# Kernel tuning notes

Hardware: AMD Instinct MI355X
Metric: run time of the kernel (lower is better)

## Reference

```python
import jax, jax.numpy as jnp
import numpy as np

N = 50000
E = 800000
IN_DIM = 16
H = 128
L = 4
EDGE_DIM = 7
LN_EPS = 1e-5


def _linear_params(key, fan_in, fan_out):
    kw, kb = jax.random.split(key)
    w = jax.random.normal(kw, (fan_in, fan_out), jnp.float32) * 0.02
    b = jax.random.normal(kb, (fan_out,), jnp.float32) * 0.02
    return w, b


def setup_inputs() -> dict:
    key = jax.random.key(0)
    ks = jax.random.split(key, 20)
    x = jax.random.normal(ks[0], (N, IN_DIM), jnp.float32)
    pos = jax.random.uniform(ks[1], (N, 3), jnp.float32) * 10.0
    row = jax.random.randint(ks[2], (E,), 0, N, jnp.int32)
    # guarantee no self-loops so distance > 0 (radius_graph uses loop=False)
    off = jax.random.randint(ks[3], (E,), 1, N, jnp.int32)
    col = (row + off) % N
    edge_index = jnp.stack([row, col], axis=0)

    W_in, b_in = _linear_params(ks[4], IN_DIM, H)

    def stack_layers(kbase, fan_in, fan_out):
        ws, bs = [], []
        for l in range(L):
            w, b = _linear_params(jax.random.fold_in(kbase, l), fan_in, fan_out)
            ws.append(w); bs.append(b)
        return jnp.stack(ws), jnp.stack(bs)

    We1, be1 = stack_layers(ks[5], 2 * H + EDGE_DIM, H)
    We2, be2 = stack_layers(ks[6], H, H)
    We3, be3 = stack_layers(ks[7], H, H)
    Wn1, bn1 = stack_layers(ks[8], H + H, H)
    Wn2, bn2 = stack_layers(ks[9], H, H)
    Wn3, bn3 = stack_layers(ks[10], H, H)
    ln_g = jnp.ones((L, H), jnp.float32)
    ln_b = jnp.zeros((L, H), jnp.float32)

    return {
        'x': x, 'pos': pos, 'edge_index': edge_index,
        'W_in': W_in, 'b_in': b_in,
        'We1': We1, 'be1': be1, 'We2': We2, 'be2': be2, 'We3': We3, 'be3': be3,
        'Wn1': Wn1, 'bn1': bn1, 'Wn2': Wn2, 'bn2': bn2, 'Wn3': Wn3, 'bn3': bn3,
        'ln_g': ln_g, 'ln_b': ln_b,
    }


def reference(x, pos, edge_index, W_in, b_in, We1, be1, We2, be2, We3, be3,
              Wn1, bn1, Wn2, bn2, Wn3, bn3, ln_g, ln_b):
    n = x.shape[0]
    row, col = edge_index[0], edge_index[1]  # row=source, col=target (PyG)
    rel_pos = pos[col] - pos[row]                       # (E, 3)
    dist = jnp.linalg.norm(rel_pos, axis=1, keepdims=True)  # (E, 1)
    edge_attr = jnp.concatenate([rel_pos, dist], axis=1)    # (E, 4)

    h = x @ W_in + b_in  # (N, H)
    num_layers = We1.shape[0]
    for l in range(num_layers):
        mom = h[:, 3:6]
        rel_mom = mom[col] - mom[row]                        # (E, 3)
        ea = jnp.concatenate([edge_attr, rel_mom], axis=1)   # (E, 7)
        # PyG: x_i = x[target=col], x_j = x[source=row]; EdgeMLP concats [h_i, h_j, ea]
        m = jnp.concatenate([h[col], h[row], ea], axis=1)    # (E, 2H+7)
        m = jax.nn.relu(m @ We1[l] + be1[l])
        m = jax.nn.relu(m @ We2[l] + be2[l])
        m = m @ We3[l] + be3[l]                              # (E, H)
        agg = jax.ops.segment_sum(m, col, num_segments=n)    # scatter-add to targets
        u = jnp.concatenate([h, agg], axis=1)                # (N, 2H)
        u = jax.nn.relu(u @ Wn1[l] + bn1[l])
        u = jax.nn.relu(u @ Wn2[l] + bn2[l])
        u = u @ Wn3[l] + bn3[l]                              # (N, H)
        h = h + u
        mean = jnp.mean(h, axis=-1, keepdims=True)
        var = jnp.mean(jnp.square(h - mean), axis=-1, keepdims=True)
        h = (h - mean) * jax.lax.rsqrt(var + LN_EPS) * ln_g[l] + ln_b[l]
    return h
```

## Files before the change

kernel.cpp:

```cpp
#include <hip/hip_runtime.h>
#include <stdint.h>

#define NN 50000
#define NE 800000
#define HD 128
#define NL 4
#define NM 64
#define EB 256

typedef __bf16 bf16x8 __attribute__((ext_vector_type(8)));
typedef __bf16 bf16x4 __attribute__((ext_vector_type(4)));
typedef float  f32x4  __attribute__((ext_vector_type(4)));

__device__ __forceinline__ f32x4 mfma16(bf16x8 a, bf16x8 b, f32x4 c) {
  return __builtin_amdgcn_mfma_f32_16x16x32_bf16(a, b, c, 0, 0, 0);
}

template<int MT, int NT>
__device__ __forceinline__ void zero_acc(f32x4 (&acc)[MT][NT]) {
#pragma unroll
  for (int i = 0; i < MT; ++i)
#pragma unroll
    for (int j = 0; j < NT; ++j) acc[i][j] = f32x4{0.f, 0.f, 0.f, 0.f};
}

template<int MT, int NT, int KS>
__device__ __forceinline__ void gemm_chunk(const __bf16* A, int sa,
    const __bf16* __restrict__ Bt, int Krow, int k0,
    int m_off, int n_off, int lane, f32x4 (&acc)[MT][NT])
{
  const int arow = lane & 15;
  const int quad = lane >> 4;
  bf16x8 b[KS][NT];
#pragma unroll
  for (int ks = 0; ks < KS; ++ks)
#pragma unroll
    for (int nt = 0; nt < NT; ++nt)
      b[ks][nt] = *reinterpret_cast<const bf16x8*>(
          Bt + (size_t)(n_off + nt * 16 + arow) * Krow + k0 + ks * 32 + quad * 8);
#pragma unroll
  for (int ks = 0; ks < KS; ++ks) {
    const int k = k0 + ks * 32 + quad * 8;
    bf16x8 a[MT];
#pragma unroll
    for (int mt = 0; mt < MT; ++mt)
      a[mt] = *reinterpret_cast<const bf16x8*>(A + (m_off + mt * 16 + arow) * sa + k);
#pragma unroll
    for (int mt = 0; mt < MT; ++mt)
#pragma unroll
      for (int nt = 0; nt < NT; ++nt)
        acc[mt][nt] = mfma16(a[mt], b[ks][nt], acc[mt][nt]);
  }
}

template<int MT, int NT, bool RELU>
__device__ __forceinline__ void store_tile(__bf16* O, int so,
    const float* __restrict__ bias, int m_off, int n_off, int lane,
    f32x4 (&acc)[MT][NT])
{
  const int quad = lane >> 4;
  const int cl = lane & 15;
#pragma unroll
  for (int nt = 0; nt < NT; ++nt) {
    const int col = n_off + nt * 16 + cl;
    const float bv = bias[col];
#pragma unroll
    for (int mt = 0; mt < MT; ++mt)
#pragma unroll
      for (int r = 0; r < 4; ++r) {
        const int row = m_off + mt * 16 + quad * 4 + r;
        float v = acc[mt][nt][r] + bv;
        if (RELU) v = fmaxf(v, 0.f);
        O[row * so + col] = (__bf16)v;
      }
  }
}

__global__ void prep_w(const float* __restrict__ W, __bf16* __restrict__ Wt,
                       int K0, int Kp) {
  int idx = blockIdx.x * 256 + threadIdx.x;
  int total = NL * HD * Kp;
  if (idx >= total) return;
  int l = idx / (HD * Kp);
  int rem = idx - l * HD * Kp;
  int n = rem / Kp;
  int k = rem - n * Kp;
  float v = (k < K0) ? W[((size_t)l * K0 + k) * HD + n] : 0.f;
  Wt[idx] = (__bf16)v;
}

__global__ void prep_pqw(const float* __restrict__ We1,
                         __bf16* __restrict__ Wtopt, __bf16* __restrict__ Wbott) {
  int idx = blockIdx.x * 256 + threadIdx.x;
  if (idx >= NL * HD * HD) return;
  int l = idx / (HD * HD);
  int rem = idx - l * HD * HD;
  int n = rem >> 7;
  int k = rem & 127;
  const float* W = We1 + (size_t)l * 263 * HD;
  float extra = (k >= 3 && k < 6) ? W[(260 + k - 3) * HD + n] : 0.f;
  Wtopt[idx] = (__bf16)(W[k * HD + n] + extra);
  Wbott[idx] = (__bf16)(W[(128 + k) * HD + n] - extra);
}

__global__ void h0_kernel(const float* __restrict__ x, const float* __restrict__ W,
                          const float* __restrict__ b, float* __restrict__ H32,
                          __bf16* __restrict__ HB) {
  int idx = blockIdx.x * 256 + threadIdx.x;
  if (idx >= NN * HD) return;
  int node = idx >> 7, j = idx & 127;
  const float* xr = x + node * 16;
  float s = b[j];
#pragma unroll
  for (int k = 0; k < 16; ++k) s += xr[k] * W[k * HD + j];
  H32[idx] = s;
  HB[idx] = (__bf16)s;
}

__global__ void hist_kernel(const int* __restrict__ ei, int* __restrict__ cnt) {
  int e = blockIdx.x * 256 + threadIdx.x;
  if (e < NE) atomicAdd(&cnt[ei[NE + e]], 1);
}

__global__ void scan_kernel(const int* __restrict__ cnt, int* __restrict__ cur) {
  __shared__ int wsum[16];
  __shared__ int carry;
  int t = threadIdx.x;
  int lane = t & 63, wid = t >> 6;
  if (t == 0) carry = 0;
  __syncthreads();
  for (int base = 0; base < NN; base += 1024) {
    int v = (base + t < NN) ? cnt[base + t] : 0;
    int incl = v;
#pragma unroll
    for (int off = 1; off < 64; off <<= 1) {
      int u = __shfl_up(incl, off, 64);
      if (lane >= off) incl += u;
    }
    if (lane == 63) wsum[wid] = incl;
    __syncthreads();
    int woff = 0;
    for (int k = 0; k < wid; ++k) woff += wsum[k];
    int c = carry;
    if (base + t < NN) cur[base + t] = c + woff + incl - v;
    __syncthreads();
    if (t == 1023) carry = c + woff + incl;
    __syncthreads();
  }
}

__global__ void scatter_kernel(const int* __restrict__ ei, int* __restrict__ cur,
                               int* __restrict__ ROWS, int* __restrict__ COLS) {
  int e = blockIdx.x * 256 + threadIdx.x;
  if (e < NE) {
    int r = ei[e], c = ei[NE + e];
    int p = atomicAdd(&cur[c], 1);
    ROWS[p] = r;
    COLS[p] = c;
  }
}

__global__ void dist_kernel(const float* __restrict__ pos,
                            const int* __restrict__ ROWS, const int* __restrict__ COLS,
                            __bf16* __restrict__ DSTb) {
  int p = blockIdx.x * 256 + threadIdx.x;
  if (p >= NE) return;
  int r = ROWS[p], c = COLS[p];
  float dx = pos[c * 3 + 0] - pos[r * 3 + 0];
  float dy = pos[c * 3 + 1] - pos[r * 3 + 1];
  float dz = pos[c * 3 + 2] - pos[r * 3 + 2];
  DSTb[p] = (__bf16)sqrtf(dx * dx + dy * dy + dz * dz);
}

__global__ __launch_bounds__(256, 4) void pq_kernel(
    const __bf16* __restrict__ HB, const float* __restrict__ pos,
    const __bf16* __restrict__ Wtopt, const __bf16* __restrict__ Wbott,
    const float* __restrict__ W4xyz,
    const float* __restrict__ be1,
    __bf16* __restrict__ PB, __bf16* __restrict__ QB)
{
  const int task = blockIdx.x * 4 + (threadIdx.x >> 6);
  const int lane = threadIdx.x & 63;
  const int g = task & 1;
  const int base = (task >> 1) * 32;
  if (base >= NN) return;
  const int arow = lane & 15, quad = lane >> 4, cl = lane & 15;

  const __bf16* Wt = g ? Wbott : Wtopt;
  __bf16* O = g ? QB : PB;
  f32x4 acc[2][8];
  zero_acc(acc);
#pragma unroll
  for (int ks = 0; ks < 4; ++ks) {
    const int k = ks * 32 + quad * 8;
    bf16x8 b[8];
#pragma unroll
    for (int nt = 0; nt < 8; ++nt)
      b[nt] = *reinterpret_cast<const bf16x8*>(Wt + (size_t)(nt * 16 + arow) * HD + k);
    bf16x8 a[2];
#pragma unroll
    for (int mt = 0; mt < 2; ++mt) {
      int row = base + mt * 16 + arow;
      if (row >= NN) row = NN - 1;
      a[mt] = *reinterpret_cast<const bf16x8*>(HB + (size_t)row * HD + k);
    }
#pragma unroll
    for (int mt = 0; mt < 2; ++mt)
#pragma unroll
      for (int nt = 0; nt < 8; ++nt)
        acc[mt][nt] = mfma16(a[mt], b[nt], acc[mt][nt]);
  }
  float px[2][4], py[2][4], pz[2][4];
#pragma unroll
  for (int mt = 0; mt < 2; ++mt)
#pragma unroll
    for (int r = 0; r < 4; ++r) {
      int row = base + mt * 16 + quad * 4 + r;
      if (row >= NN) row = NN - 1;
      px[mt][r] = pos[row * 3 + 0];
      py[mt][r] = pos[row * 3 + 1];
      pz[mt][r] = pos[row * 3 + 2];
    }
#pragma unroll
  for (int nt = 0; nt < 8; ++nt) {
    const int col = nt * 16 + cl;
    const float w0 = W4xyz[col], w1 = W4xyz[HD + col], w2 = W4xyz[2 * HD + col];
    const float bb = g ? 0.f : be1[col];
#pragma unroll
    for (int mt = 0; mt < 2; ++mt)
#pragma unroll
      for (int r = 0; r < 4; ++r) {
        const int row = base + mt * 16 + quad * 4 + r;
        if (row < NN) {
          float dot = px[mt][r] * w0 + py[mt][r] * w1 + pz[mt][r] * w2;
          float v = acc[mt][nt][r] + (g ? -dot : dot) + bb;
          O[(size_t)row * HD + col] = (__bf16)v;
        }
      }
  }
}

__global__ __launch_bounds__(512, 4) void edge_kernel(
    const __bf16* __restrict__ PB, const __bf16* __restrict__ QB,
    const __bf16* __restrict__ DSTb,
    const int* __restrict__ ROWS, const int* __restrict__ COLS,
    const float* __restrict__ w4d,
    const __bf16* __restrict__ We2t, const __bf16* __restrict__ We3t,
    const float* __restrict__ be2, const float* __restrict__ be3,
    float* __restrict__ AGG)
{
  __shared__ __bf16 S[EB * 136];
  __shared__ float w4ds[HD], be2s[HD], be3s[HD];
  __shared__ int colS[EB];
  __shared__ unsigned long long bmaskS[EB / 64];
  const int t = threadIdx.x;

  const int nwg = gridDim.x;
  const int q = nwg >> 3, r8 = nwg & 7;
  const int xcd = blockIdx.x & 7, idx8 = blockIdx.x >> 3;
  const int bswz = (xcd < r8 ? xcd * (q + 1) : r8 * (q + 1) + (xcd - r8) * q) + idx8;
  const int base = bswz * EB;

  if (t < HD) { w4ds[t] = w4d[t]; be2s[t] = be2[t]; be3s[t] = be3[t]; }
  if (t < EB) colS[t] = COLS[base + t];
  __syncthreads();

  if (t < EB) {
    int d = (t == EB - 1) || (colS[t + 1] != colS[t]);
    unsigned long long bm = __ballot(d);
    if ((t & 63) == 0) bmaskS[t >> 6] = bm;
  }

  {
    const int i0 = t >> 2, cg = t & 3;
#pragma unroll
    for (int g2 = 0; g2 < 2; ++g2) {
      const int i = g2 * 128 + i0;
      const int p = base + i;
      const int c = colS[i];
      const int r = ROWS[p];
      const float dist = (float)DSTb[p];
      const __bf16* Prow = PB + (size_t)c * HD;
      const __bf16* Qrow = QB + (size_t)r * HD;
#pragma unroll
      for (int u = 0; u < 4; ++u) {
        const int ch = cg * 4 + u;
        bf16x8 pv = *reinterpret_cast<const bf16x8*>(Prow + ch * 8);
        bf16x8 qv = *reinterpret_cast<const bf16x8*>(Qrow + ch * 8);
        bf16x8 o;
#pragma unroll
        for (int j = 0; j < 8; ++j) {
          const int col = ch * 8 + j;
          float f = (float)pv[j] + (float)qv[j] + dist * w4ds[col];
          o[j] = (__bf16)fmaxf(f, 0.f);
        }
        *reinterpret_cast<bf16x8*>(S + i * 136 + ch * 8) = o;
      }
    }
  }
  __syncthreads();

  const int w = t >> 6, lane = t & 63;
  const int m_off = (w >> 1) * 64, n_off = (w & 1) * 64;
  const int arow = lane & 15, quad = lane >> 4, cl = lane & 15;

  f32x4 acc[4][4];
#pragma unroll
  for (int g = 0; g < 2; ++g) {
    const __bf16* Wt = g ? We3t : We2t;
    const float* bs = g ? be3s : be2s;
    zero_acc(acc);
#pragma unroll
    for (int half = 0; half < 2; ++half) {
      bf16x8 b[2][4];
#pragma unroll
      for (int ks = 0; ks < 2; ++ks)
#pragma unroll
        for (int nt = 0; nt < 4; ++nt)
          b[ks][nt] = *reinterpret_cast<const bf16x8*>(
              Wt + (size_t)(n_off + nt * 16 + arow) * HD + half * 64 + ks * 32 + quad * 8);
#pragma unroll
      for (int ks = 0; ks < 2; ++ks) {
        const int k = half * 64 + ks * 32 + quad * 8;
        bf16x8 a[4];
#pragma unroll
        for (int mt = 0; mt < 4; ++mt)
          a[mt] = *reinterpret_cast<const bf16x8*>(S + (m_off + mt * 16 + arow) * 136 + k);
#pragma unroll
        for (int mt = 0; mt < 4; ++mt)
#pragma unroll
          for (int nt = 0; nt < 4; ++nt)
            acc[mt][nt] = mfma16(a[mt], b[ks][nt], acc[mt][nt]);
      }
    }
    __syncthreads();
#pragma unroll
    for (int nt = 0; nt < 4; ++nt) {
      const int col = n_off + nt * 16 + cl;
      const float bv = bs[col];
#pragma unroll
      for (int mt = 0; mt < 4; ++mt)
#pragma unroll
        for (int r = 0; r < 4; ++r) {
          const int row = m_off + mt * 16 + quad * 4 + r;
          float v = acc[mt][nt][r] + bv;
          if (!g) v = fmaxf(v, 0.f);
          S[row * 136 + col] = (__bf16)v;
        }
    }
    __syncthreads();
  }

  {
    const int j = t & 127, qtr = t >> 7;
    const int i0 = qtr * 64;
    unsigned long long m = bmaskS[qtr] | (1ull << 63);
    float s = 0.f;
    for (int i = i0; i < i0 + 64; ++i) {
      s += (float)S[i * 136 + j];
      if ((m >> (i - i0)) & 1ull) {
        atomicAdd(&AGG[(size_t)colS[i] * HD + j], s);
        s = 0.f;
      }
    }
  }
}

__global__ __launch_bounds__(256, 4) void node_kernel(
    const __bf16* __restrict__ HBin, float* __restrict__ AGG,
    const __bf16* __restrict__ Wn1t, const __bf16* __restrict__ Wn2t,
    const __bf16* __restrict__ Wn3t,
    const float* __restrict__ bn1, const float* __restrict__ bn2,
    const float* __restrict__ bn3,
    const float* __restrict__ lng, const float* __restrict__ lnb,
    float* __restrict__ H32, __bf16* __restrict__ HBout,
    float* __restrict__ dout)
{
  __shared__ float SB[NM * 136];
  __shared__ float ps[NM][2], psq[NM][2];
  __shared__ float mean_s[NM], rstd_s[NM];
  __bf16* B16 = reinterpret_cast<__bf16*>(SB);
  const int t = threadIdx.x;
  const int base = blockIdx.x * NM;

  {
    const int i0 = t >> 4, s = t & 15;
#pragma unroll
    for (int g = 0; g < NM / 16; ++g) {
      const int i = g * 16 + i0;
      const int node = base + i;
      uint4 v = make_uint4(0, 0, 0, 0);
      if (node < NN) v = *(reinterpret_cast<const uint4*>(HBin + (size_t)node * HD) + s);
      *reinterpret_cast<uint4*>(&B16[i * 264 + s * 8]) = v;
    }
  }
  for (int idx = t; idx < NM * 32; idx += 256) {
    const int i = idx >> 5, c4 = idx & 31;
    const int node = base + i;
    float4 v = make_float4(0.f, 0.f, 0.f, 0.f);
    if (node < NN) {
      float4* ap = reinterpret_cast<float4*>(AGG + (size_t)node * HD + c4 * 4);
      v = *ap;
      *ap = make_float4(0.f, 0.f, 0.f, 0.f);
    }
    __bf16* d = &B16[i * 264 + HD + c4 * 4];
    d[0] = (__bf16)v.x; d[1] = (__bf16)v.y; d[2] = (__bf16)v.z; d[3] = (__bf16)v.w;
  }
  __syncthreads();

  const int w = t >> 6, lane = t & 63;
  const int m_off = (w >> 1) * 32, n_off = (w & 1) * 64;
  f32x4 acc[2][4];
  __bf16* reg0 = B16;
  __bf16* reg1 = B16 + NM * 136;

  zero_acc(acc);
  gemm_chunk<2, 4, 4>(B16, 264, Wn1t, 256, 0,   m_off, n_off, lane, acc);
  gemm_chunk<2, 4, 4>(B16, 264, Wn1t, 256, 128, m_off, n_off, lane, acc);
  __syncthreads();
  store_tile<2, 4, true>(reg0, 136, bn1, m_off, n_off, lane, acc);
  __syncthreads();
  zero_acc(acc);
  gemm_chunk<2, 4, 4>(reg0, 136, Wn2t, 128, 0, m_off, n_off, lane, acc);
  store_tile<2, 4, true>(reg1, 136, bn2, m_off, n_off, lane, acc);
  __syncthreads();
  zero_acc(acc);
  gemm_chunk<2, 4, 4>(reg1, 136, Wn3t, 128, 0, m_off, n_off, lane, acc);
  __syncthreads();

  {
    const int quad = lane >> 4, cl = lane & 15;
#pragma unroll
    for (int nt = 0; nt < 4; ++nt) {
      const int col = n_off + nt * 16 + cl;
      const float bv = bn3[col];
#pragma unroll
      for (int mt = 0; mt < 2; ++mt)
#pragma unroll
        for (int r = 0; r < 4; ++r) {
          const int row = m_off + mt * 16 + quad * 4 + r;
          const int node = base + row;
          float hv = (node < NN) ? H32[(size_t)node * HD + col] : 0.f;
          SB[row * 136 + col] = hv + acc[mt][nt][r] + bv;
        }
    }
  }
  __syncthreads();
  if (t < 128) {
    const int r = t >> 1, hh = t & 1;
    float s = 0.f, sq = 0.f;
    for (int j = hh * 64; j < hh * 64 + 64; ++j) {
      float v = SB[r * 136 + j];
      s += v; sq += v * v;
    }
    ps[r][hh] = s; psq[r][hh] = sq;
  }
  __syncthreads();
  if (t < NM) {
    float s = ps[t][0] + ps[t][1];
    float sq = psq[t][0] + psq[t][1];
    float mean = s * (1.f / HD);
    float var = sq * (1.f / HD) - mean * mean;
    mean_s[t] = mean;
    rstd_s[t] = rsqrtf(var + 1e-5f);
  }
  __syncthreads();
  for (int idx = t; idx < NM * HD; idx += 256) {
    const int r = idx >> 7, j = idx & 127;
    const int node = base + r;
    if (node < NN) {
      float v = (SB[r * 136 + j] - mean_s[r]) * rstd_s[r] * lng[j] + lnb[j];
      H32[(size_t)node * HD + j] = v;
      HBout[(size_t)node * HD + j] = (__bf16)v;
      if (dout) dout[(size_t)node * HD + j] = v;
    }
  }
}

extern "C" void kernel_launch(void* const* d_in, const int* in_sizes, int n_in,
                              void* d_out, int out_size, void* d_ws, size_t ws_size,
                              hipStream_t stream)
{
  const float* x    = (const float*)d_in[0];
  const float* pos  = (const float*)d_in[1];
  const int*   ei   = (const int*)d_in[2];
  const float* W_in = (const float*)d_in[3];
  const float* b_in = (const float*)d_in[4];
  const float* We1  = (const float*)d_in[5];
  const float* be1  = (const float*)d_in[6];
  const float* We2  = (const float*)d_in[7];
  const float* be2  = (const float*)d_in[8];
  const float* We3  = (const float*)d_in[9];
  const float* be3  = (const float*)d_in[10];
  const float* Wn1  = (const float*)d_in[11];
  const float* bn1  = (const float*)d_in[12];
  const float* Wn2  = (const float*)d_in[13];
  const float* bn2  = (const float*)d_in[14];
  const float* Wn3  = (const float*)d_in[15];
  const float* bn3  = (const float*)d_in[16];
  const float* lng  = (const float*)d_in[17];
  const float* lnb  = (const float*)d_in[18];
  float* out = (float*)d_out;

  char* ws = (char*)d_ws;
  size_t off = 0;
  auto alloc = [&](size_t bytes) -> char* {
    char* p = ws + off;
    off += (bytes + 255) & ~(size_t)255;
    return p;
  };
  __bf16* Wtopt = (__bf16*)alloc((size_t)NL * HD * HD * 2);
  __bf16* Wbott = (__bf16*)alloc((size_t)NL * HD * HD * 2);
  __bf16* We2t = (__bf16*)alloc((size_t)NL * HD * HD * 2);
  __bf16* We3t = (__bf16*)alloc((size_t)NL * HD * HD * 2);
  __bf16* Wn1t = (__bf16*)alloc((size_t)NL * HD * 256 * 2);
  __bf16* Wn2t = (__bf16*)alloc((size_t)NL * HD * HD * 2);
  __bf16* Wn3t = (__bf16*)alloc((size_t)NL * HD * HD * 2);
  __bf16* DSTb = (__bf16*)alloc((size_t)NE * 2);
  float*  H32  = (float*) alloc((size_t)NN * HD * 4);
  __bf16* HB   = (__bf16*)alloc((size_t)NN * HD * 2);
  __bf16* PB   = (__bf16*)alloc((size_t)NN * HD * 2);
  __bf16* QB   = (__bf16*)alloc((size_t)NN * HD * 2);
  float*  AGG  = (float*) alloc((size_t)NN * HD * 4);
  int*    CNT  = (int*)   alloc((size_t)NN * 4);
  int*    CUR  = (int*)   alloc((size_t)NN * 4);
  int*    ROWS = (int*)   alloc((size_t)NE * 4);
  int*    COLS = (int*)   alloc((size_t)NE * 4);

  hipMemsetAsync(CNT, 0, (size_t)NN * 4, stream);
  hipMemsetAsync(AGG, 0, (size_t)NN * HD * 4, stream);
  prep_pqw<<<(NL * HD * HD + 255) / 256, 256, 0, stream>>>(We1, Wtopt, Wbott);
  prep_w<<<(NL * HD * HD + 255) / 256, 256, 0, stream>>>(We2, We2t, 128, 128);
  prep_w<<<(NL * HD * HD + 255) / 256, 256, 0, stream>>>(We3, We3t, 128, 128);
  prep_w<<<(NL * HD * 256 + 255) / 256, 256, 0, stream>>>(Wn1, Wn1t, 256, 256);
  prep_w<<<(NL * HD * HD + 255) / 256, 256, 0, stream>>>(Wn2, Wn2t, 128, 128);
  prep_w<<<(NL * HD * HD + 255) / 256, 256, 0, stream>>>(Wn3, Wn3t, 128, 128);
  h0_kernel<<<(NN * HD + 255) / 256, 256, 0, stream>>>(x, W_in, b_in, H32, HB);
  hist_kernel<<<(NE + 255) / 256, 256, 0, stream>>>(ei, CNT);
  scan_kernel<<<1, 1024, 0, stream>>>(CNT, CUR);
  scatter_kernel<<<(NE + 255) / 256, 256, 0, stream>>>(ei, CUR, ROWS, COLS);
  dist_kernel<<<(NE + 255) / 256, 256, 0, stream>>>(pos, ROWS, COLS, DSTb);

  const int pq_tasks = 2 * ((NN + 31) / 32);
  const int pq_blocks = (pq_tasks + 3) / 4;
  for (int l = 0; l < NL; ++l) {
    const float* We1l = We1 + (size_t)l * 263 * HD;
    pq_kernel<<<pq_blocks, 256, 0, stream>>>(HB, pos,
        Wtopt + (size_t)l * HD * HD, Wbott + (size_t)l * HD * HD,
        We1l + 256 * HD,
        be1 + l * HD, PB, QB);
    edge_kernel<<<NE / EB, 512, 0, stream>>>(PB, QB, DSTb, ROWS, COLS,
        We1l + 259 * HD,
        We2t + (size_t)l * HD * HD, We3t + (size_t)l * HD * HD,
        be2 + l * HD, be3 + l * HD, AGG);
    node_kernel<<<(NN + NM - 1) / NM, 256, 0, stream>>>(HB, AGG,
        Wn1t + (size_t)l * HD * 256, Wn2t + (size_t)l * HD * HD,
        Wn3t + (size_t)l * HD * HD,
        bn1 + l * HD, bn2 + l * HD, bn3 + l * HD,
        lng + l * HD, lnb + l * HD,
        H32, HB, (l == NL - 1) ? out : nullptr);
  }
}
```

Measured before the change: 1.300 ms.

## Halve edge tile, double-buffer LDS across edge MLP layers, retile MFMA warps

The edge kernel now handles 128 edges per workgroup instead of 256. The single LDS activation buffer becomes two ping-pong buffers, so the barrier between the MFMA reads and the write-back of each layer can be dropped. Warps are retiled to 64x32 output blocks and preload the full weight K-range for their columns. The intent is to cut barrier stalls and raise parallelism, at the cost of twice as many workgroups, more per-block setup, and more atomic flushes at tile boundaries.

```diff
diff --git a/kernel.cpp b/kernel.cpp
--- a/kernel.cpp
+++ b/kernel.cpp
@@ -6,7 +6,7 @@
 #define HD 128
 #define NL 4
 #define NM 64
-#define EB 256
+#define EB 128
 
 typedef __bf16 bf16x8 __attribute__((ext_vector_type(8)));
 typedef __bf16 bf16x4 __attribute__((ext_vector_type(4)));
@@ -249,7 +249,8 @@
     const float* __restrict__ be2, const float* __restrict__ be3,
     float* __restrict__ AGG)
 {
-  __shared__ __bf16 S[EB * 136];
+  __shared__ __bf16 S1[EB * 136];
+  __shared__ __bf16 S2[EB * 136];
   __shared__ float w4ds[HD], be2s[HD], be3s[HD];
   __shared__ int colS[EB];
   __shared__ unsigned long long bmaskS[EB / 64];
@@ -272,70 +273,66 @@
   }
 
   {
-    const int i0 = t >> 2, cg = t & 3;
-#pragma unroll
-    for (int g2 = 0; g2 < 2; ++g2) {
-      const int i = g2 * 128 + i0;
-      const int p = base + i;
-      const int c = colS[i];
-      const int r = ROWS[p];
-      const float dist = (float)DSTb[p];
-      const __bf16* Prow = PB + (size_t)c * HD;
-      const __bf16* Qrow = QB + (size_t)r * HD;
-#pragma unroll
-      for (int u = 0; u < 4; ++u) {
-        const int ch = cg * 4 + u;
-        bf16x8 pv = *reinterpret_cast<const bf16x8*>(Prow + ch * 8);
-        bf16x8 qv = *reinterpret_cast<const bf16x8*>(Qrow + ch * 8);
-        bf16x8 o;
-#pragma unroll
-        for (int j = 0; j < 8; ++j) {
-          const int col = ch * 8 + j;
-          float f = (float)pv[j] + (float)qv[j] + dist * w4ds[col];
-          o[j] = (__bf16)fmaxf(f, 0.f);
-        }
-        *reinterpret_cast<bf16x8*>(S + i * 136 + ch * 8) = o;
+    const int i = t >> 2, cg = t & 3;
+    const int p = base + i;
+    const int c = colS[i];
+    const int r = ROWS[p];
+    const float dist = (float)DSTb[p];
+    const __bf16* Prow = PB + (size_t)c * HD;
+    const __bf16* Qrow = QB + (size_t)r * HD;
+#pragma unroll
+    for (int u = 0; u < 4; ++u) {
+      const int ch = cg * 4 + u;
+      bf16x8 pv = *reinterpret_cast<const bf16x8*>(Prow + ch * 8);
+      bf16x8 qv = *reinterpret_cast<const bf16x8*>(Qrow + ch * 8);
+      bf16x8 o;
+#pragma unroll
+      for (int j = 0; j < 8; ++j) {
+        const int col = ch * 8 + j;
+        float f = (float)pv[j] + (float)qv[j] + dist * w4ds[col];
+        o[j] = (__bf16)fmaxf(f, 0.f);
       }
+      *reinterpret_cast<bf16x8*>(S1 + i * 136 + ch * 8) = o;
     }
   }
   __syncthreads();
 
   const int w = t >> 6, lane = t & 63;
-  const int m_off = (w >> 1) * 64, n_off = (w & 1) * 64;
+  const int m_off = (w >> 2) * 64, n_off = (w & 3) * 32;
   const int arow = lane & 15, quad = lane >> 4, cl = lane & 15;
 
-  f32x4 acc[4][4];
+  f32x4 acc[4][2];
 #pragma unroll
   for (int g = 0; g < 2; ++g) {
     const __bf16* Wt = g ? We3t : We2t;
     const float* bs = g ? be3s : be2s;
+    const __bf16* Sin  = g ? S2 : S1;
+    __bf16* Sout = g ? S1 : S2;
+
+    bf16x8 b[4][2];
+#pragma unroll
+    for (int ks = 0; ks < 4; ++ks)
+#pragma unroll
+      for (int nt = 0; nt < 2; ++nt)
+        b[ks][nt] = *reinterpret_cast<const bf16x8*>(
+            Wt + (size_t)(n_off + nt * 16 + arow) * HD + ks * 32 + quad * 8);
+
     zero_acc(acc);
 #pragma unroll
-    for (int half = 0; half < 2; ++half) {
-      bf16x8 b[2][4];
-#pragma unroll
-      for (int ks = 0; ks < 2; ++ks)
-#pragma unroll
-        for (int nt = 0; nt < 4; ++nt)
-          b[ks][nt] = *reinterpret_cast<const bf16x8*>(
-              Wt + (size_t)(n_off + nt * 16 + arow) * HD + half * 64 + ks * 32 + quad * 8);
-#pragma unroll
-      for (int ks = 0; ks < 2; ++ks) {
-        const int k = half * 64 + ks * 32 + quad * 8;
-        bf16x8 a[4];
-#pragma unroll
-        for (int mt = 0; mt < 4; ++mt)
-          a[mt] = *reinterpret_cast<const bf16x8*>(S + (m_off + mt * 16 + arow) * 136 + k);
-#pragma unroll
-        for (int mt = 0; mt < 4; ++mt)
-#pragma unroll
-          for (int nt = 0; nt < 4; ++nt)
-            acc[mt][nt] = mfma16(a[mt], b[ks][nt], acc[mt][nt]);
-      }
-    }
-    __syncthreads();
-#pragma unroll
-    for (int nt = 0; nt < 4; ++nt) {
+    for (int ks = 0; ks < 4; ++ks) {
+      const int k = ks * 32 + quad * 8;
+      bf16x8 a[4];
+#pragma unroll
+      for (int mt = 0; mt < 4; ++mt)
+        a[mt] = *reinterpret_cast<const bf16x8*>(Sin + (m_off + mt * 16 + arow) * 136 + k);
+#pragma unroll
+      for (int mt = 0; mt < 4; ++mt)
+#pragma unroll
+        for (int nt = 0; nt < 2; ++nt)
+          acc[mt][nt] = mfma16(a[mt], b[ks][nt], acc[mt][nt]);
+    }
+#pragma unroll
+    for (int nt = 0; nt < 2; ++nt) {
       const int col = n_off + nt * 16 + cl;
       const float bv = bs[col];
 #pragma unroll
@@ -345,7 +342,7 @@
           const int row = m_off + mt * 16 + quad * 4 + r;
           float v = acc[mt][nt][r] + bv;
           if (!g) v = fmaxf(v, 0.f);
-          S[row * 136 + col] = (__bf16)v;
+          Sout[row * 136 + col] = (__bf16)v;
         }
     }
     __syncthreads();
@@ -353,12 +350,14 @@
 
   {
     const int j = t & 127, qtr = t >> 7;
-    const int i0 = qtr * 64;
-    unsigned long long m = bmaskS[qtr] | (1ull << 63);
+    const int i0 = qtr * 32;
+    unsigned int m = (unsigned int)(bmaskS[qtr >> 1] >> ((qtr & 1) * 32));
+    m |= 0x80000000u;
     float s = 0.f;
-    for (int i = i0; i < i0 + 64; ++i) {
-      s += (float)S[i * 136 + j];
-      if ((m >> (i - i0)) & 1ull) {
+    for (int r = 0; r < 32; ++r) {
+      const int i = i0 + r;
+      s += (float)S1[i * 136 + j];
+      if ((m >> r) & 1u) {
         atomicAdd(&AGG[(size_t)colS[i] * HD + j], s);
         s = 0.f;
       }
```

Result: faster. 1.242 ms (-4.4%).
